# Optimization experiments

Hardware: AMD Instinct MI355X
Metric: run time of the kernel (lower is better)

Reference implementation:

```python
import jax, jax.numpy as jnp
import numpy as np

GRID = (8, 8)
EPS = 1e-5  # nn.BatchNorm2d default eps


def _per_tile(t, g, b, w, cb):
    # t: (B, C, th, tw); training-mode BatchNorm over (B, th, tw) per channel
    mean = t.mean(axis=(0, 2, 3))
    var = t.var(axis=(0, 2, 3))  # biased variance, matches torch BN normalization
    xn = (t - mean[:, None, None]) * jax.lax.rsqrt(var[:, None, None] + EPS)
    h = jax.nn.relu(xn * g[:, None, None] + b[:, None, None])
    y = jax.lax.conv_general_dilated(
        h, w, window_strides=(1, 1), padding='SAME',
        dimension_numbers=('NCHW', 'OIHW', 'NCHW'))
    return y + cb[:, None, None] + t  # conv bias + residual


def setup_inputs() -> dict:
    key = jax.random.key(0)
    k1, k2 = jax.random.split(key)
    B, C, H, W = 32, 32, 160, 160
    n_tiles = GRID[0] * GRID[1]
    x = jax.random.normal(k1, (B, C, H, W), dtype=jnp.float32)
    gamma = jnp.ones((n_tiles, C), dtype=jnp.float32)
    beta = jnp.zeros((n_tiles, C), dtype=jnp.float32)
    # kaiming-ish init for 3x3 conv
    conv_w = jax.random.normal(k2, (n_tiles, C, C, 3, 3), dtype=jnp.float32) * (2.0 / (C * 9)) ** 0.5
    conv_b = jnp.zeros((n_tiles, C), dtype=jnp.float32)
    return {"x": x, "gamma": gamma, "beta": beta, "conv_w": conv_w, "conv_b": conv_b}


def reference(x, gamma, beta, conv_w, conv_b):
    B, C, H, W = x.shape
    gi, gj = GRID
    th, tw = H // gi, W // gj
    # split into (gi*gj, B, C, th, tw) tiles
    tiles = x.reshape(B, C, gi, th, gj, tw).transpose(2, 4, 0, 1, 3, 5)
    tiles = tiles.reshape(gi * gj, B, C, th, tw)
    out = jax.vmap(_per_tile)(tiles, gamma, beta, conv_w, conv_b)
    # reassemble
    out = out.reshape(gi, gj, B, C, th, tw).transpose(2, 3, 0, 4, 1, 5)
    return out.reshape(B, C, H, W)
```

## Files before the change

### kernel.cpp

```cpp
#include <hip/hip_runtime.h>

#define NT 64
#define B_ 32
#define C_ 32
#define H_ 160
#define W_ 160
#define TH 20
#define TW 20
#define NPIX (TH*TW)
#define NRED (B_*NPIX)
#define EPS 1e-5f

#define HP 40
#define OP 404

typedef __bf16 bf16x8 __attribute__((ext_vector_type(8)));
typedef __bf16 bf16x4 __attribute__((ext_vector_type(4)));
typedef float  f32x4  __attribute__((ext_vector_type(4)));

__global__ __launch_bounds__(320) void statsA_kernel(const float* __restrict__ x,
                                                     float* __restrict__ ppS,
                                                     float* __restrict__ ppS2) {
    int blk = blockIdx.x;
    int b = blk >> 5;
    int c = blk & 31;
    const float* plane = x + ((long)(b*C_ + c)) * H_ * W_;

    int tid   = threadIdx.x;
    int col4  = tid % 40;
    int rbase = tid / 40;

    __shared__ float sh [8 * 321];
    __shared__ float sh2[8 * 321];

    #pragma unroll
    for (int tr = 0; tr < 8; ++tr) {
        float s = 0.f, s2 = 0.f;
        #pragma unroll
        for (int k = 0; k < 3; ++k) {
            int r20 = rbase + 8*k;
            if (r20 < 20) {
                int row = tr*20 + r20;
                float4 v = *(const float4*)(plane + row*W_ + col4*4);
                s  += v.x + v.y + v.z + v.w;
                s2 += v.x*v.x + v.y*v.y + v.z*v.z + v.w*v.w;
            }
        }
        sh [tr*321 + tid] = s;
        sh2[tr*321 + tid] = s2;
    }
    __syncthreads();

    if (tid < 64) {
        int tr = tid >> 3, tc = tid & 7;
        float ps = 0.f, ps2 = 0.f;
        #pragma unroll
        for (int rb = 0; rb < 8; ++rb)
            #pragma unroll
            for (int c5 = 0; c5 < 5; ++c5) {
                int t = tr*321 + rb*40 + tc*5 + c5;
                ps += sh[t]; ps2 += sh2[t];
            }
        int tl = tr*8 + tc;
        atomicAdd(&ppS [tl*C_ + c], ps);
        atomicAdd(&ppS2[tl*C_ + c], ps2);
    }
}

__global__ __launch_bounds__(512, 4) void fused_kernel(
        const float* __restrict__ x,
        const float* __restrict__ gamma,
        const float* __restrict__ beta,
        const float* __restrict__ conv_w,
        const float* __restrict__ conv_b,
        const float* __restrict__ ppS,
        const float* __restrict__ ppS2,
        float* __restrict__ out) {
    int blk = blockIdx.x;
    int tl = blk >> 5;
    int b  = blk & 31;
    int ti = (tl >> 3) * TH;
    int tj = (tl & 7)  * TW;
    int tid = threadIdx.x;

    __shared__ __align__(16) unsigned char smem[64832];
    __bf16* hlds   = (__bf16*)smem;
    __bf16* wlds   = (__bf16*)(smem + 38720);
    __bf16* obuf   = (__bf16*)(smem + 38720);
    float*  scale  = (float*)(smem + 64576);
    float*  shiftv = (float*)(smem + 64704);

    {
        uint4* hz = (uint4*)smem;
        for (int i = tid; i < 2420; i += 512) hz[i] = uint4{0,0,0,0};
    }
    if (tid < C_) {
        int c = tid;
        float s   = ppS [tl*C_ + c];
        float s2  = ppS2[tl*C_ + c];
        float m   = s / (float)NRED;
        float var = s2 / (float)NRED - m*m;
        float rs  = rsqrtf(var + EPS);
        float g   = gamma[tl*C_ + c];
        scale[c]  = g * rs;
        shiftv[c] = beta[tl*C_ + c] - m * rs * g;
    }
    {
        const float* wsrc = conv_w + (long)tl * C_ * C_ * 9;
        for (int f = tid; f < C_*C_*9; f += 512) {
            int co  = f / 288;
            int rem = f - co*288;
            int cin = rem / 9;
            int tap = rem - cin*9;
            wlds[(tap*C_ + co)*HP + cin] = (__bf16)wsrc[f];
        }
    }
    __syncthreads();

    for (int idx = tid; idx < C_*TH*5; idx += 512) {
        int c   = idx / 100;
        int rem = idx - c*100;
        int y   = rem / 5;
        int x4  = rem - y*5;
        const float* p = x + ((long)(b*C_ + c)*H_ + ti + y)*W_ + tj + x4*4;
        float4 v = *(const float4*)p;
        float sc = scale[c], sf = shiftv[c];
        int base = ((y+1)*22 + (x4*4 + 1)) * HP + c;
        hlds[base         ] = (__bf16)fmaxf(v.x*sc + sf, 0.f);
        hlds[base +   HP  ] = (__bf16)fmaxf(v.y*sc + sf, 0.f);
        hlds[base + 2*HP  ] = (__bf16)fmaxf(v.z*sc + sf, 0.f);
        hlds[base + 3*HP  ] = (__bf16)fmaxf(v.w*sc + sf, 0.f);
    }
    __syncthreads();

    int lane = tid & 63;
    int wv   = tid >> 6;
    int mm   = lane & 15;
    int jg   = lane >> 4;
    int j0   = jg * 8;

    bf16x8 bfr[9][2];
    #pragma unroll
    for (int tap = 0; tap < 9; ++tap) {
        #pragma unroll
        for (int h = 0; h < 2; ++h)
            bfr[tap][h] = *(const bf16x8*)&wlds[(tap*C_ + (h*16 + mm))*HP + j0];
    }
    float b0 = conv_b[tl*C_ + mm];
    float b1 = conv_b[tl*C_ + 16 + mm];
    __syncthreads();

    for (int chunk = wv; chunk < 25; chunk += 8) {
        int p  = chunk*16 + mm;
        int py = p / 20;
        int px = p - py*20;
        f32x4 a0, a1;
        #pragma unroll
        for (int r = 0; r < 4; ++r) { a0[r] = b0; a1[r] = b1; }
        #pragma unroll
        for (int ky = 0; ky < 3; ++ky) {
            #pragma unroll
            for (int kx = 0; kx < 3; ++kx) {
                bf16x8 af = *(const bf16x8*)&hlds[((py+ky)*22 + (px+kx))*HP + j0];
                a0 = __builtin_amdgcn_mfma_f32_16x16x32_bf16(af, bfr[ky*3+kx][0], a0, 0, 0, 0);
                a1 = __builtin_amdgcn_mfma_f32_16x16x32_bf16(af, bfr[ky*3+kx][1], a1, 0, 0, 0);
            }
        }
        bf16x4 o0, o1;
        #pragma unroll
        for (int r = 0; r < 4; ++r) { o0[r] = (__bf16)a0[r]; o1[r] = (__bf16)a1[r]; }
        int pb = chunk*16 + jg*4;
        *(bf16x4*)&obuf[mm*OP + pb]        = o0;
        *(bf16x4*)&obuf[(16 + mm)*OP + pb] = o1;
    }
    __syncthreads();

    for (int idx = tid; idx < C_*NPIX/4; idx += 512) {
        int co = idx / 100;
        int q  = idx - co*100;
        int y  = q / 5;
        int x4 = q - y*5;
        bf16x4 v = *(const bf16x4*)&obuf[co*OP + y*20 + x4*4];
        long o = (((long)(b*C_ + co))*H_ + ti + y)*W_ + tj + x4*4;
        float4 xr = *(const float4*)&x[o];
        float4 ov;
        ov.x = (float)v[0] + xr.x;
        ov.y = (float)v[1] + xr.y;
        ov.z = (float)v[2] + xr.z;
        ov.w = (float)v[3] + xr.w;
        *(float4*)&out[o] = ov;
    }
}

extern "C" void kernel_launch(void* const* d_in, const int* in_sizes, int n_in,
                              void* d_out, int out_size, void* d_ws, size_t ws_size,
                              hipStream_t stream) {
    const float* x      = (const float*)d_in[0];
    const float* gamma  = (const float*)d_in[1];
    const float* beta   = (const float*)d_in[2];
    const float* conv_w = (const float*)d_in[3];
    const float* conv_b = (const float*)d_in[4];
    float* out = (float*)d_out;

    float* ppS  = (float*)d_ws;
    float* ppS2 = ppS + NT*C_;

    hipMemsetAsync(d_ws, 0, 2 * NT * C_ * sizeof(float), stream);
    statsA_kernel<<<B_ * C_, 320, 0, stream>>>(x, ppS, ppS2);
    fused_kernel<<<NT * B_, 512, 0, stream>>>(x, gamma, beta, conv_w, conv_b,
                                              ppS, ppS2, out);
}
```

Before: 273.8 us.

## Write conv output directly from MFMA accumulators, zero only halo, gather channel-packed loads

The LDS output staging buffer and its extra barrier are removed. Each wave now adds the residual to its MFMA accumulators in fp32 and writes them straight to global memory. Only the halo border of the padded activation tile is zeroed instead of the whole buffer, and the activation fill gathers 8 channels per pixel into a single 16-byte LDS store. Weights are read from LDS per tap with a padded row stride instead of being held in registers, and each wave works on three chunks at once to increase MFMA independence. Global stores become scattered float4 writes spread across channel planes, and the output no longer goes through a bf16 rounding of the conv result.

```diff
diff --git a/kernel.cpp b/kernel.cpp
--- a/kernel.cpp
+++ b/kernel.cpp
@@ -12,10 +12,9 @@
 #define EPS 1e-5f
 
 #define HP 40
-#define OP 404
+#define WSL 33
 
 typedef __bf16 bf16x8 __attribute__((ext_vector_type(8)));
-typedef __bf16 bf16x4 __attribute__((ext_vector_type(4)));
 typedef float  f32x4  __attribute__((ext_vector_type(4)));
 
 __global__ __launch_bounds__(320) void statsA_kernel(const float* __restrict__ x,
@@ -83,16 +82,20 @@
     int tj = (tl & 7)  * TW;
     int tid = threadIdx.x;
 
-    __shared__ __align__(16) unsigned char smem[64832];
+    __shared__ __align__(16) unsigned char smem[62656];
     __bf16* hlds   = (__bf16*)smem;
     __bf16* wlds   = (__bf16*)(smem + 38720);
-    __bf16* obuf   = (__bf16*)(smem + 38720);
-    float*  scale  = (float*)(smem + 64576);
-    float*  shiftv = (float*)(smem + 64704);
-
-    {
-        uint4* hz = (uint4*)smem;
-        for (int i = tid; i < 2420; i += 512) hz[i] = uint4{0,0,0,0};
+    float*  scale  = (float*)(smem + 62400);
+    float*  shiftv = (float*)(smem + 62528);
+
+    if (tid < 420) {
+        int hp = tid / 5, q = tid - hp*5;
+        int P;
+        if      (hp < 22) P = hp;
+        else if (hp < 44) P = 462 + (hp - 22);
+        else if (hp < 64) P = (hp - 43) * 22;
+        else              P = (hp - 63) * 22 + 21;
+        ((uint4*)smem)[P*5 + q] = uint4{0,0,0,0};
     }
     if (tid < C_) {
         int c = tid;
@@ -106,30 +109,32 @@
         shiftv[c] = beta[tl*C_ + c] - m * rs * g;
     }
     {
-        const float* wsrc = conv_w + (long)tl * C_ * C_ * 9;
+        const float* wsrc = conv_w + (long)tl * (C_*C_*9);
         for (int f = tid; f < C_*C_*9; f += 512) {
             int co  = f / 288;
             int rem = f - co*288;
             int cin = rem / 9;
             int tap = rem - cin*9;
-            wlds[(tap*C_ + co)*HP + cin] = (__bf16)wsrc[f];
+            wlds[(tap*WSL + co)*HP + cin] = (__bf16)wsrc[f];
         }
     }
     __syncthreads();
 
-    for (int idx = tid; idx < C_*TH*5; idx += 512) {
-        int c   = idx / 100;
-        int rem = idx - c*100;
-        int y   = rem / 5;
-        int x4  = rem - y*5;
-        const float* p = x + ((long)(b*C_ + c)*H_ + ti + y)*W_ + tj + x4*4;
-        float4 v = *(const float4*)p;
-        float sc = scale[c], sf = shiftv[c];
-        int base = ((y+1)*22 + (x4*4 + 1)) * HP + c;
-        hlds[base         ] = (__bf16)fmaxf(v.x*sc + sf, 0.f);
-        hlds[base +   HP  ] = (__bf16)fmaxf(v.y*sc + sf, 0.f);
-        hlds[base + 2*HP  ] = (__bf16)fmaxf(v.z*sc + sf, 0.f);
-        hlds[base + 3*HP  ] = (__bf16)fmaxf(v.w*sc + sf, 0.f);
+    for (int idx = tid; idx < 4*NPIX; idx += 512) {
+        int cg = idx / NPIX;
+        int p  = idx - cg*NPIX;
+        int y  = p / 20;
+        int xx = p - y*20;
+        int c0 = cg*8;
+        const float* ps = x + (((long)(b*C_ + c0)*H_ + ti + y)*W_ + tj + xx);
+        float v[8];
+        #pragma unroll
+        for (int k = 0; k < 8; ++k) v[k] = ps[k * (H_*W_)];
+        bf16x8 h;
+        #pragma unroll
+        for (int k = 0; k < 8; ++k)
+            h[k] = (__bf16)fmaxf(v[k]*scale[c0+k] + shiftv[c0+k], 0.f);
+        *(bf16x8*)&hlds[((y+1)*22 + xx + 1)*HP + c0] = h;
     }
     __syncthreads();
 
@@ -138,57 +143,69 @@
     int mm   = lane & 15;
     int jg   = lane >> 4;
     int j0   = jg * 8;
-
-    bf16x8 bfr[9][2];
-    #pragma unroll
-    for (int tap = 0; tap < 9; ++tap) {
-        #pragma unroll
-        for (int h = 0; h < 2; ++h)
-            bfr[tap][h] = *(const bf16x8*)&wlds[(tap*C_ + (h*16 + mm))*HP + j0];
-    }
     float b0 = conv_b[tl*C_ + mm];
     float b1 = conv_b[tl*C_ + 16 + mm];
-    __syncthreads();
-
-    for (int chunk = wv; chunk < 25; chunk += 8) {
-        int p  = chunk*16 + mm;
+
+    auto store_chunk = [&](int chunk, f32x4 a0, f32x4 a1) {
+        int pb = chunk*16 + jg*4;
+        int py = pb / 20;
+        int px = pb - py*20;
+        long o0 = ((long)(b*C_ + mm)*H_ + ti + py)*W_ + tj + px;
+        long o1 = o0 + (long)16*H_*W_;
+        float4 x0 = *(const float4*)&x[o0];
+        float4 x1 = *(const float4*)&x[o1];
+        float4 r0 = make_float4(a0[0]+x0.x, a0[1]+x0.y, a0[2]+x0.z, a0[3]+x0.w);
+        float4 r1 = make_float4(a1[0]+x1.x, a1[1]+x1.y, a1[2]+x1.z, a1[3]+x1.w);
+        *(float4*)&out[o0] = r0;
+        *(float4*)&out[o1] = r1;
+    };
+
+    const __bf16* ab[3];
+    #pragma unroll
+    for (int i = 0; i < 3; ++i) {
+        int p  = (wv + 8*i)*16 + mm;
         int py = p / 20;
         int px = p - py*20;
-        f32x4 a0, a1;
-        #pragma unroll
-        for (int r = 0; r < 4; ++r) { a0[r] = b0; a1[r] = b1; }
-        #pragma unroll
-        for (int ky = 0; ky < 3; ++ky) {
-            #pragma unroll
-            for (int kx = 0; kx < 3; ++kx) {
-                bf16x8 af = *(const bf16x8*)&hlds[((py+ky)*22 + (px+kx))*HP + j0];
-                a0 = __builtin_amdgcn_mfma_f32_16x16x32_bf16(af, bfr[ky*3+kx][0], a0, 0, 0, 0);
-                a1 = __builtin_amdgcn_mfma_f32_16x16x32_bf16(af, bfr[ky*3+kx][1], a1, 0, 0, 0);
-            }
-        }
-        bf16x4 o0, o1;
-        #pragma unroll
-        for (int r = 0; r < 4; ++r) { o0[r] = (__bf16)a0[r]; o1[r] = (__bf16)a1[r]; }
-        int pb = chunk*16 + jg*4;
-        *(bf16x4*)&obuf[mm*OP + pb]        = o0;
-        *(bf16x4*)&obuf[(16 + mm)*OP + pb] = o1;
-    }
-    __syncthreads();
-
-    for (int idx = tid; idx < C_*NPIX/4; idx += 512) {
-        int co = idx / 100;
-        int q  = idx - co*100;
-        int y  = q / 5;
-        int x4 = q - y*5;
-        bf16x4 v = *(const bf16x4*)&obuf[co*OP + y*20 + x4*4];
-        long o = (((long)(b*C_ + co))*H_ + ti + y)*W_ + tj + x4*4;
-        float4 xr = *(const float4*)&x[o];
-        float4 ov;
-        ov.x = (float)v[0] + xr.x;
-        ov.y = (float)v[1] + xr.y;
-        ov.z = (float)v[2] + xr.z;
-        ov.w = (float)v[3] + xr.w;
-        *(float4*)&out[o] = ov;
+        ab[i] = &hlds[(py*22 + px)*HP + j0];
+    }
+    f32x4 acc[3][2];
+    #pragma unroll
+    for (int i = 0; i < 3; ++i) {
+        acc[i][0] = f32x4{b0,b0,b0,b0};
+        acc[i][1] = f32x4{b1,b1,b1,b1};
+    }
+    #pragma unroll
+    for (int tap = 0; tap < 9; ++tap) {
+        const int ky = tap/3, kx = tap - (tap/3)*3;
+        bf16x8 w0 = *(const bf16x8*)&wlds[(tap*WSL + mm)*HP + j0];
+        bf16x8 w1 = *(const bf16x8*)&wlds[(tap*WSL + 16 + mm)*HP + j0];
+        #pragma unroll
+        for (int i = 0; i < 3; ++i) {
+            bf16x8 af = *(const bf16x8*)(ab[i] + (ky*22 + kx)*HP);
+            acc[i][0] = __builtin_amdgcn_mfma_f32_16x16x32_bf16(af, w0, acc[i][0], 0, 0, 0);
+            acc[i][1] = __builtin_amdgcn_mfma_f32_16x16x32_bf16(af, w1, acc[i][1], 0, 0, 0);
+        }
+    }
+    #pragma unroll
+    for (int i = 0; i < 3; ++i) store_chunk(wv + 8*i, acc[i][0], acc[i][1]);
+
+    if (wv == 0) {
+        int p  = 24*16 + mm;
+        int py = p / 20;
+        int px = p - py*20;
+        const __bf16* a3 = &hlds[(py*22 + px)*HP + j0];
+        f32x4 c0v = f32x4{b0,b0,b0,b0};
+        f32x4 c1v = f32x4{b1,b1,b1,b1};
+        #pragma unroll
+        for (int tap = 0; tap < 9; ++tap) {
+            const int ky = tap/3, kx = tap - (tap/3)*3;
+            bf16x8 w0 = *(const bf16x8*)&wlds[(tap*WSL + mm)*HP + j0];
+            bf16x8 w1 = *(const bf16x8*)&wlds[(tap*WSL + 16 + mm)*HP + j0];
+            bf16x8 af = *(const bf16x8*)(a3 + (ky*22 + kx)*HP);
+            c0v = __builtin_amdgcn_mfma_f32_16x16x32_bf16(af, w0, c0v, 0, 0, 0);
+            c1v = __builtin_amdgcn_mfma_f32_16x16x32_bf16(af, w1, c1v, 0, 0, 0);
+        }
+        store_chunk(24, c0v, c1v);
     }
 }
 
```

Result: no change. 271.5 us (-0.8%).
